# Optimization experiments

Hardware: AMD Instinct MI355X
Metric: run time of the kernel (lower is better)

Reference implementation:

```python
import jax, jax.numpy as jnp
import numpy as np
import math
from functools import partial

B = 256
H = 256
HEADS = 4
DK = H // HEADS
NA_MAX, NP_MAX, NH_MAX = 127, 23, 11


def _counts():
    i = np.arange(B)
    ac = (64 + i % 64).astype(np.int32)   # atoms per graph, 64..127
    pc = (8 + i % 16).astype(np.int32)    # pharm fragments per graph, 8..23
    hc = (4 + i % 8).astype(np.int32)     # hyper-edges per graph, 4..11
    return ac, pc, hc


def setup_inputs() -> dict:
    key = jax.random.key(0)
    ks = jax.random.split(key, 32)
    ac, pc, hc = _counts()
    na, npm, nh = int(ac.sum()), int(pc.sum()), int(hc.sum())
    w = 1.0 / math.sqrt(H)
    inp = {
        'atom_message': jax.random.normal(ks[0], (na, H), jnp.float32),
        'pharm_message': jax.random.normal(ks[1], (npm, H), jnp.float32),
        'hyper_message': jax.random.normal(ks[2], (nh, H), jnp.float32),
        'atom_counts': jnp.asarray(ac),
        'pharm_counts': jnp.asarray(pc),
        'hyper_counts': jnp.asarray(hc),
    }
    # two MultiHeadedAttention blocks: q/k/v/out linears each (W stored as [in, out])
    names = []
    for pre in ('p2h', 'a2p'):
        for part in ('Wq', 'bq', 'Wk', 'bk', 'Wv', 'bv', 'Wo', 'bo'):
            names.append(f'{pre}_{part}')
    ki = 3
    for n in names:
        if n.split('_')[1].startswith('W'):
            inp[n] = jax.random.normal(ks[ki], (H, H), jnp.float32) * w
        else:
            inp[n] = jax.random.normal(ks[ki], (H,), jnp.float32) * 0.01
        ki += 1
    # bidirectional GRU params, torch layout: W_ih [3H, H], W_hh [3H, H], b [3H]
    for d in ('f', 'b'):
        inp[f'gru_Wih_{d}'] = jax.random.normal(ks[ki], (3 * H, H), jnp.float32) * w; ki += 1
        inp[f'gru_Whh_{d}'] = jax.random.normal(ks[ki], (3 * H, H), jnp.float32) * w; ki += 1
        inp[f'gru_bih_{d}'] = jax.random.normal(ks[ki], (3 * H,), jnp.float32) * 0.01; ki += 1
        inp[f'gru_bhh_{d}'] = jax.random.normal(ks[ki], (3 * H,), jnp.float32) * 0.01; ki += 1
    return inp


def _split_pad(msg, counts, max_n):
    # faithful vectorized version of split_batch: narrow + zero-pad per graph
    starts = jnp.concatenate([jnp.zeros((1,), jnp.int32), jnp.cumsum(counts)[:-1].astype(jnp.int32)])
    j = jnp.arange(max_n)
    valid = j[None, :] < counts[:, None]                       # [B, max_n]
    idx = jnp.where(valid, starts[:, None] + j[None, :], msg.shape[0])
    padded_src = jnp.concatenate([msg, jnp.zeros((1, msg.shape[1]), msg.dtype)], 0)
    return padded_src[idx], valid                              # [B, max_n, H]


def _mha(q, k, v, mask, Wq, bq, Wk, bk, Wv, bv, Wo, bo):
    Bq, Lq, _ = q.shape
    def proj(x, W, b):
        y = x @ W + b
        return y.reshape(x.shape[0], x.shape[1], HEADS, DK).transpose(0, 2, 1, 3)
    qh, kh, vh = proj(q, Wq, bq), proj(k, Wk, bk), proj(v, Wv, bv)
    scores = jnp.einsum('bhqd,bhkd->bhqk', qh, kh) / math.sqrt(DK)
    scores = jnp.where(mask[:, None], jnp.float32(-1e9), scores)
    p = jax.nn.softmax(scores, axis=-1)
    o = jnp.einsum('bhqk,bhkd->bhqd', p, vh)
    o = o.transpose(0, 2, 1, 3).reshape(Bq, Lq, H)
    return o @ Wo + bo


def _gru_dir(x, h0, Wih, Whh, bih, bhh):
    # x: [B, T, H], torch GRU cell equations
    def step(h, xt):
        gi = xt @ Wih.T + bih
        gh = h @ Whh.T + bhh
        ir, iz, inn = jnp.split(gi, 3, axis=-1)
        hr, hz, hn = jnp.split(gh, 3, axis=-1)
        r = jax.nn.sigmoid(ir + hr)
        z = jax.nn.sigmoid(iz + hz)
        n = jnp.tanh(inn + r * hn)
        h = (1.0 - z) * n + z * h
        return h, h
    _, ys = jax.lax.scan(step, h0, x.transpose(1, 0, 2))
    return ys.transpose(1, 0, 2)


def reference(atom_message, pharm_message, hyper_message,
              p2h_Wq, p2h_bq, p2h_Wk, p2h_bk, p2h_Wv, p2h_bv, p2h_Wo, p2h_bo,
              a2p_Wq, a2p_bq, a2p_Wk, a2p_bk, a2p_Wv, a2p_bv, a2p_Wo, a2p_bo,
              gru_Wih_f, gru_Whh_f, gru_bih_f, gru_bhh_f,
              gru_Wih_b, gru_Whh_b, gru_bih_b, gru_bhh_b,
              atom_counts, pharm_counts, hyper_counts):
    atom_f, atom_valid = _split_pad(atom_message, atom_counts, NA_MAX)
    pharm_f, _ = _split_pad(pharm_message, pharm_counts, NP_MAX)
    hyper_f, _ = _split_pad(hyper_message, hyper_counts, NH_MAX)

    nz = lambda t: (t != 0).astype(jnp.float32)
    mask1 = jnp.einsum('bqh,bkh->bqk', nz(pharm_f), nz(hyper_f)) == 0  # [B, Np, Nh]
    mask2 = jnp.einsum('bqh,bkh->bqk', nz(atom_f), nz(pharm_f)) == 0   # [B, Na, Np]

    pharm_f = _mha(pharm_f, hyper_f, hyper_f, mask1,
                   p2h_Wq, p2h_bq, p2h_Wk, p2h_bk, p2h_Wv, p2h_bv, p2h_Wo, p2h_bo) + pharm_f
    h = _mha(atom_f, pharm_f, pharm_f, mask2,
             a2p_Wq, a2p_bq, a2p_Wk, a2p_bk, a2p_Wv, a2p_bv, a2p_Wo, a2p_bo) + atom_f

    h0 = h.max(axis=1)  # initial hidden per direction
    hf = _gru_dir(h, h0, gru_Wih_f, gru_Whh_f, gru_bih_f, gru_bhh_f)
    hb = _gru_dir(h[:, ::-1], h0, gru_Wih_b, gru_Whh_b, gru_bih_b, gru_bhh_b)[:, ::-1]
    hcat = jnp.concatenate([hf, hb], axis=-1)  # [B, Na, 2H]

    v = atom_valid.astype(hcat.dtype)[..., None]
    graph_embed = (hcat * v).sum(axis=1) / atom_counts[:, None].astype(hcat.dtype)
    return graph_embed  # [B, 2H]
```

## Files before the change

### kernel.cpp

```cpp
#include <hip/hip_runtime.h>
#include <hip/hip_fp16.h>
#include <math.h>

#define NB 256
#define HDIM 256
#define NHEADS 4
#define DKH 64
#define LA 127
#define LP 23
#define LH 11

typedef _Float16 h2v __attribute__((ext_vector_type(2)));
typedef _Float16 f16x8 __attribute__((ext_vector_type(8)));
typedef float f32x4 __attribute__((ext_vector_type(4)));
union F4H { float4 f4; h2v h[4]; };

__device__ __forceinline__ float dot2acc(h2v a, h2v b, float c) {
#if __has_builtin(__builtin_amdgcn_fdot2)
  return __builtin_amdgcn_fdot2(a, b, c, false);
#else
  return c + (float)a[0] * (float)b[0] + (float)a[1] * (float)b[1];
#endif
}

__device__ __forceinline__ float sigm(float x) { return 1.0f / (1.0f + __expf(-x)); }
__device__ __forceinline__ float tanh_fast(float x) { return 2.0f / (1.0f + __expf(-2.0f * x)) - 1.0f; }

__global__ void k_prep(const int* __restrict__ ac, const int* __restrict__ pc,
                       const int* __restrict__ hc, int* __restrict__ sa,
                       int* __restrict__ sp, int* __restrict__ sh,
                       const float* __restrict__ Whh_f, __half* __restrict__ Wh16_f,
                       const float* __restrict__ Whh_b, __half* __restrict__ Wh16_b,
                       const float* __restrict__ Wih_f, __half* __restrict__ Wf16_f,
                       const float* __restrict__ Wih_b, __half* __restrict__ Wf16_b,
                       const float* __restrict__ Wq, __half* __restrict__ Wqh,
                       __half* __restrict__ Wql, const float* __restrict__ Wo,
                       __half* __restrict__ Woh, __half* __restrict__ Wol) {
  const int NT = 768 * 256, NP = 256 * 256;
  if (blockIdx.x == gridDim.x - 1) {
    int t = threadIdx.x;
    if (t == 0) { int s = 0; for (int i = 0; i < NB; i++) { sa[i] = s; s += ac[i]; } }
    else if (t == 1) { int s = 0; for (int i = 0; i < NB; i++) { sp[i] = s; s += pc[i]; } }
    else if (t == 2) { int s = 0; for (int i = 0; i < NB; i++) { sh[i] = s; s += hc[i]; } }
    return;
  }
  int idx = blockIdx.x * 256 + threadIdx.x;
  if (idx < NT) { Wh16_f[idx] = __float2half(Whh_f[idx]); return; }
  idx -= NT;
  if (idx < NT) { Wh16_b[idx] = __float2half(Whh_b[idx]); return; }
  idx -= NT;
  if (idx < NT) {
    int u = idx & 7, lg = (idx >> 3) & 3, c = (idx >> 5) % 768, k0b = (idx >> 5) / 768;
    Wf16_f[idx] = __float2half(Wih_f[(size_t)c * 256 + k0b * 32 + lg * 8 + u]);
    return;
  }
  idx -= NT;
  if (idx < NT) {
    int u = idx & 7, lg = (idx >> 3) & 3, c = (idx >> 5) % 768, k0b = (idx >> 5) / 768;
    Wf16_b[idx] = __float2half(Wih_b[(size_t)c * 256 + k0b * 32 + lg * 8 + u]);
    return;
  }
  idx -= NT;
  if (idx < NP) {
    int u = idx & 7, lg = (idx >> 3) & 3, c = (idx >> 5) & 255, k0b = idx >> 13;
    float w = Wq[(size_t)(k0b * 32 + lg * 8 + u) * 256 + c];
    __half h = __float2half(w);
    Wqh[idx] = h; Wql[idx] = __float2half(w - __half2float(h));
    return;
  }
  idx -= NP;
  if (idx < NP) {
    int u = idx & 7, lg = (idx >> 3) & 3, c = (idx >> 5) & 255, k0b = idx >> 13;
    float w = Wo[(size_t)(k0b * 32 + lg * 8 + u) * 256 + c];
    __half h = __float2half(w);
    Woh[idx] = h; Wol[idx] = __float2half(w - __half2float(h));
  }
}

__global__ void k_gsplit(const float* __restrict__ msg, const int* __restrict__ starts,
                         const int* __restrict__ counts, int L, int M,
                         __half* __restrict__ hi, __half* __restrict__ lo) {
  int idx = blockIdx.x * blockDim.x + threadIdx.x;
  if (idx >= M * 256) return;
  int r = idx >> 8, c = idx & 255;
  int b = r / L, t = r - b * L;
  float v = (t < counts[b]) ? msg[(size_t)(starts[b] + t) * 256 + c] : 0.f;
  __half h = __float2half(v);
  hi[idx] = h;
  lo[idx] = __float2half(v - __half2float(h));
}

template <bool GATHER_A, bool RES_GATHER>
__global__ __launch_bounds__(256) void k_gemm(
    const float* __restrict__ A, const float* __restrict__ msg,
    const int* __restrict__ starts, const int* __restrict__ counts, int L,
    const float* __restrict__ W, const float* __restrict__ bias,
    const float* __restrict__ resmsg, float* __restrict__ C,
    __half* __restrict__ Ch, int N) {
  const int K = HDIM;
  __shared__ float As[16][76];
  __shared__ float Ws[16][72];
  int tid = threadIdx.x;
  int row0 = blockIdx.x * 64, col0 = blockIdx.y * 64;
  int arow = row0 + (tid >> 2);
  const float* asrc;
  if constexpr (GATHER_A) {
    int b = arow / L, t = arow - b * L;
    asrc = (t < counts[b]) ? (msg + (size_t)(starts[b] + t) * K) : nullptr;
  } else {
    asrc = A + (size_t)arow * K;
  }
  int ak = (tid & 3) * 4;
  int wk = tid >> 4, wn = (tid & 15) * 4;
  int ty = tid >> 4, tx = tid & 15;
  float acc[4][4] = {};
  for (int k0 = 0; k0 < K; k0 += 16) {
    float4 av = make_float4(0.f, 0.f, 0.f, 0.f);
    if (asrc) av = *(const float4*)(asrc + k0 + ak);
    float4 wv = *(const float4*)(W + (size_t)(k0 + wk) * N + col0 + wn);
    __syncthreads();
    int m = tid >> 2;
    As[ak + 0][m] = av.x; As[ak + 1][m] = av.y;
    As[ak + 2][m] = av.z; As[ak + 3][m] = av.w;
    *(float4*)&Ws[wk][wn] = wv;
    __syncthreads();
#pragma unroll
    for (int kk = 0; kk < 16; kk++) {
      float4 a = *(const float4*)&As[kk][ty * 4];
      float4 b = *(const float4*)&Ws[kk][tx * 4];
      acc[0][0] += a.x * b.x; acc[0][1] += a.x * b.y; acc[0][2] += a.x * b.z; acc[0][3] += a.x * b.w;
      acc[1][0] += a.y * b.x; acc[1][1] += a.y * b.y; acc[1][2] += a.y * b.z; acc[1][3] += a.y * b.w;
      acc[2][0] += a.z * b.x; acc[2][1] += a.z * b.y; acc[2][2] += a.z * b.z; acc[2][3] += a.z * b.w;
      acc[3][0] += a.w * b.x; acc[3][1] += a.w * b.y; acc[3][2] += a.w * b.z; acc[3][3] += a.w * b.w;
    }
  }
  float4 bv = *(const float4*)(bias + col0 + tx * 4);
#pragma unroll
  for (int i = 0; i < 4; i++) {
    int r = row0 + ty * 4 + i;
    float o0 = acc[i][0] + bv.x, o1 = acc[i][1] + bv.y,
          o2 = acc[i][2] + bv.z, o3 = acc[i][3] + bv.w;
    if constexpr (RES_GATHER) {
      int b = r / L, t = r - b * L;
      if (t < counts[b]) {
        float4 rv = *(const float4*)(resmsg + (size_t)(starts[b] + t) * K + col0 + tx * 4);
        o0 += rv.x; o1 += rv.y; o2 += rv.z; o3 += rv.w;
      }
    }
    size_t o = (size_t)r * N + col0 + tx * 4;
    *(float4*)(C + o) = make_float4(o0, o1, o2, o3);
    if (Ch) {
      Ch[o] = __float2half(o0); Ch[o + 1] = __float2half(o1);
      Ch[o + 2] = __float2half(o2); Ch[o + 3] = __float2half(o3);
    }
  }
}

template <bool GATHER_A>
__global__ __launch_bounds__(256) void k_gemm_kv(
    const float* __restrict__ A, const float* __restrict__ msg,
    const int* __restrict__ starts, const int* __restrict__ counts, int L,
    const float* __restrict__ W0, const float* __restrict__ b0, float* __restrict__ C0,
    const float* __restrict__ W1, const float* __restrict__ b1, float* __restrict__ C1) {
  const int K = HDIM, N = HDIM;
  const float* W = blockIdx.z ? W1 : W0;
  const float* bias = blockIdx.z ? b1 : b0;
  float* C = blockIdx.z ? C1 : C0;
  __shared__ float As[16][76];
  __shared__ float Ws[16][72];
  int tid = threadIdx.x;
  int row0 = blockIdx.x * 64, col0 = blockIdx.y * 64;
  int arow = row0 + (tid >> 2);
  const float* asrc;
  if constexpr (GATHER_A) {
    int b = arow / L, t = arow - b * L;
    asrc = (t < counts[b]) ? (msg + (size_t)(starts[b] + t) * K) : nullptr;
  } else {
    asrc = A + (size_t)arow * K;
  }
  int ak = (tid & 3) * 4;
  int wk = tid >> 4, wn = (tid & 15) * 4;
  int ty = tid >> 4, tx = tid & 15;
  float acc[4][4] = {};
  for (int k0 = 0; k0 < K; k0 += 16) {
    float4 av = make_float4(0.f, 0.f, 0.f, 0.f);
    if (asrc) av = *(const float4*)(asrc + k0 + ak);
    float4 wv = *(const float4*)(W + (size_t)(k0 + wk) * N + col0 + wn);
    __syncthreads();
    int m = tid >> 2;
    As[ak + 0][m] = av.x; As[ak + 1][m] = av.y;
    As[ak + 2][m] = av.z; As[ak + 3][m] = av.w;
    *(float4*)&Ws[wk][wn] = wv;
    __syncthreads();
#pragma unroll
    for (int kk = 0; kk < 16; kk++) {
      float4 a = *(const float4*)&As[kk][ty * 4];
      float4 b = *(const float4*)&Ws[kk][tx * 4];
      acc[0][0] += a.x * b.x; acc[0][1] += a.x * b.y; acc[0][2] += a.x * b.z; acc[0][3] += a.x * b.w;
      acc[1][0] += a.y * b.x; acc[1][1] += a.y * b.y; acc[1][2] += a.y * b.z; acc[1][3] += a.y * b.w;
      acc[2][0] += a.z * b.x; acc[2][1] += a.z * b.y; acc[2][2] += a.z * b.z; acc[2][3] += a.z * b.w;
      acc[3][0] += a.w * b.x; acc[3][1] += a.w * b.y; acc[3][2] += a.w * b.z; acc[3][3] += a.w * b.w;
    }
  }
  float4 bv = *(const float4*)(bias + col0 + tx * 4);
#pragma unroll
  for (int i = 0; i < 4; i++) {
    int r = row0 + ty * 4 + i;
    size_t o = (size_t)r * N + col0 + tx * 4;
    *(float4*)(C + o) = make_float4(acc[i][0] + bv.x, acc[i][1] + bv.y,
                                    acc[i][2] + bv.z, acc[i][3] + bv.w);
  }
}

template <bool RES>
__global__ __launch_bounds__(256) void k_mfma_sp(
    const __half* __restrict__ Ahi, const __half* __restrict__ Alo,
    const __half* __restrict__ Whi, const __half* __restrict__ Wlo,
    const float* __restrict__ bias, const float* __restrict__ resmsg,
    const int* __restrict__ starts, const int* __restrict__ counts, int L,
    float* __restrict__ Out, __half* __restrict__ Ch) {
  int w = threadIdx.x >> 6, l = threadIdx.x & 63;
  int row0 = blockIdx.x * 64 + w * 16;
  int col0 = blockIdx.y * 64;
  int lr = l & 15, lg = l >> 4;
  f32x4 acc[4] = {};
  const __half* ahrow = Ahi + (size_t)(row0 + lr) * 256 + lg * 8;
  const __half* alrow = Alo + (size_t)(row0 + lr) * 256 + lg * 8;
#pragma unroll
  for (int k0b = 0; k0b < 8; k0b++) {
    f16x8 ah = *(const f16x8*)(ahrow + k0b * 32);
    f16x8 al = *(const f16x8*)(alrow + k0b * 32);
#pragma unroll
    for (int nt = 0; nt < 4; nt++) {
      int c = col0 + nt * 16 + lr;
      size_t wi = ((size_t)(k0b * 256 + c) * 4 + lg) * 8;
      f16x8 bh = *(const f16x8*)(Whi + wi);
      f16x8 bl = *(const f16x8*)(Wlo + wi);
      acc[nt] = __builtin_amdgcn_mfma_f32_16x16x32_f16(ah, bh, acc[nt], 0, 0, 0);
      acc[nt] = __builtin_amdgcn_mfma_f32_16x16x32_f16(al, bh, acc[nt], 0, 0, 0);
      acc[nt] = __builtin_amdgcn_mfma_f32_16x16x32_f16(ah, bl, acc[nt], 0, 0, 0);
    }
  }
#pragma unroll
  for (int nt = 0; nt < 4; nt++) {
    int c = col0 + nt * 16 + lr;
    float bv = bias[c];
#pragma unroll
    for (int r = 0; r < 4; r++) {
      int row = row0 + lg * 4 + r;
      float o = acc[nt][r] + bv;
      if constexpr (RES) {
        int b = row / L, t = row - b * L;
        if (t < counts[b]) o += resmsg[(size_t)(starts[b] + t) * 256 + c];
      }
      size_t oidx = (size_t)row * 256 + c;
      Out[oidx] = o;
      if (Ch) Ch[oidx] = __float2half(o);
    }
  }
}

__global__ __launch_bounds__(256) void k_mfma_gi2(
    const __half* __restrict__ A16,
    const __half* __restrict__ Wf_f, const __half* __restrict__ Wf_b,
    const float* __restrict__ bias_f, const float* __restrict__ bias_b,
    __half* __restrict__ Out_f, __half* __restrict__ Out_b) {
  const int N = 768;
  int y = blockIdx.y;
  const __half* Wf = y < 12 ? Wf_f : Wf_b;
  const float* bias = y < 12 ? bias_f : bias_b;
  __half* Out = y < 12 ? Out_f : Out_b;
  int col0 = (y < 12 ? y : y - 12) * 64;
  int w = threadIdx.x >> 6, l = threadIdx.x & 63;
  int row0 = blockIdx.x * 64 + w * 16;
  int lr = l & 15, lg = l >> 4;
  f32x4 acc[4] = {};
  const __half* arow = A16 + (size_t)(row0 + lr) * 256 + lg * 8;
#pragma unroll
  for (int k0b = 0; k0b < 8; k0b++) {
    f16x8 a = *(const f16x8*)(arow + k0b * 32);
#pragma unroll
    for (int nt = 0; nt < 4; nt++) {
      int c = col0 + nt * 16 + lr;
      f16x8 b = *(const f16x8*)(Wf + ((size_t)(k0b * N + c) * 4 + lg) * 8);
      acc[nt] = __builtin_amdgcn_mfma_f32_16x16x32_f16(a, b, acc[nt], 0, 0, 0);
    }
  }
#pragma unroll
  for (int nt = 0; nt < 4; nt++) {
    int c = col0 + nt * 16 + lr;
    float bv = bias[c];
#pragma unroll
    for (int r = 0; r < 4; r++) {
      int row = row0 + lg * 4 + r;
      Out[(size_t)row * N + c] = __float2half(acc[nt][r] + bv);
    }
  }
}

template <int LQ, int LK, bool SPLITOUT>
__global__ __launch_bounds__(128) void k_attn(
    float* __restrict__ q, const float* __restrict__ kbuf,
    const float* __restrict__ vbuf, const int* __restrict__ cq,
    const int* __restrict__ ck, __half* __restrict__ oh, __half* __restrict__ ol) {
  __shared__ float qs[LQ][65];
  __shared__ float ks[LK][65];
  __shared__ float vs[LK][65];
  int b = blockIdx.x, head = blockIdx.y;
  int tid = threadIdx.x;
  for (int idx = tid; idx < LQ * 16; idx += 128) {
    int i = idx >> 4, c = (idx & 15) * 4;
    float4 v = *(const float4*)(q + (size_t)(b * LQ + i) * HDIM + head * DKH + c);
    qs[i][c] = v.x; qs[i][c + 1] = v.y; qs[i][c + 2] = v.z; qs[i][c + 3] = v.w;
  }
  for (int idx = tid; idx < LK * 16; idx += 128) {
    int i = idx >> 4, c = (idx & 15) * 4;
    float4 v = *(const float4*)(kbuf + (size_t)(b * LK + i) * HDIM + head * DKH + c);
    ks[i][c] = v.x; ks[i][c + 1] = v.y; ks[i][c + 2] = v.z; ks[i][c + 3] = v.w;
    float4 w = *(const float4*)(vbuf + (size_t)(b * LK + i) * HDIM + head * DKH + c);
    vs[i][c] = w.x; vs[i][c + 1] = w.y; vs[i][c + 2] = w.z; vs[i][c + 3] = w.w;
  }
  __syncthreads();
  int nq = cq[b], nk = ck[b];
  for (int i = tid; i < LQ; i += 128) {
    float4 qr[16];
#pragma unroll
    for (int c4 = 0; c4 < 16; c4++) qr[c4] = *(const float4*)&qs[i][c4 * 4];
    float s[LK];
    float mx = -INFINITY;
    bool qv = i < nq;
#pragma unroll
    for (int k = 0; k < LK; k++) {
      float d = -1e9f;
      if (qv && k < nk) {
        float acc = 0.f;
#pragma unroll
        for (int c4 = 0; c4 < 16; c4++) {
          float4 kv = *(const float4*)&ks[k][c4 * 4];
          acc += qr[c4].x * kv.x + qr[c4].y * kv.y + qr[c4].z * kv.z + qr[c4].w * kv.w;
        }
        d = acc * 0.125f;
      }
      s[k] = d;
      mx = fmaxf(mx, d);
    }
    float den = 0.f;
#pragma unroll
    for (int k = 0; k < LK; k++) { s[k] = expf(s[k] - mx); den += s[k]; }
    float inv = 1.0f / den;
#pragma unroll
    for (int c4 = 0; c4 < 16; c4++) {
      float4 a = make_float4(0.f, 0.f, 0.f, 0.f);
#pragma unroll
      for (int k = 0; k < LK; k++) {
        float4 vv = *(const float4*)&vs[k][c4 * 4];
        a.x += s[k] * vv.x; a.y += s[k] * vv.y;
        a.z += s[k] * vv.z; a.w += s[k] * vv.w;
      }
      a.x *= inv; a.y *= inv; a.z *= inv; a.w *= inv;
      size_t o = (size_t)(b * LQ + i) * HDIM + head * DKH + c4 * 4;
      *(float4*)(q + o) = a;
      if constexpr (SPLITOUT) {
        float vals[4] = {a.x, a.y, a.z, a.w};
#pragma unroll
        for (int u = 0; u < 4; u++) {
          __half h = __float2half(vals[u]);
          oh[o + u] = h;
          ol[o + u] = __float2half(vals[u] - __half2float(h));
        }
      }
    }
  }
}

__global__ __launch_bounds__(512, 2) void k_gru4(
    const float* __restrict__ h_x, const __half* __restrict__ Wh_f,
    const __half* __restrict__ Wh_b, const __half* __restrict__ gi_f,
    const __half* __restrict__ gi_b, const float* __restrict__ bhh_f,
    const float* __restrict__ bhh_b, const int* __restrict__ ac,
    float* __restrict__ out) {
  int bid = blockIdx.x;
  int dir = bid & 1, pair = bid >> 1;
  int g0 = pair, g1 = pair + 128;
  int tid = threadIdx.x;
  int j = tid >> 1, half = tid & 1;
  const __half* W = dir ? Wh_b : Wh_f;
  const __half* gih = dir ? gi_b : gi_f;
  const float* bhh = dir ? bhh_b : bhh_f;

  __shared__ float h0s[2][HDIM];
  {
    int g = tid >> 8, jj = tid & 255;
    int gg = g ? g1 : g0;
    const float* hp_ = h_x + (size_t)gg * LA * HDIM + jj;
    float m = -INFINITY;
    for (int t = 0; t < LA; t++) m = fmaxf(m, hp_[(size_t)t * HDIM]);
    h0s[g][jj] = m;
  }

  F4H wr[16], wz[16], wn[16];
  {
    const float4* Wr4 = (const float4*)(W + (size_t)j * 256 + half * 128);
    const float4* Wz4 = (const float4*)(W + (size_t)(256 + j) * 256 + half * 128);
    const float4* Wn4 = (const float4*)(W + (size_t)(512 + j) * 256 + half * 128);
#pragma unroll
    for (int p = 0; p < 16; p++) wr[p].f4 = Wr4[p];
#pragma unroll
    for (int p = 0; p < 16; p++) wz[p].f4 = Wz4[p];
#pragma unroll
    for (int p = 0; p < 16; p++) wn[p].f4 = Wn4[p];
  }
  float br = bhh[j], bz = bhh[256 + j], bn = bhh[512 + j];
  int cnt = ac[g0];

  __syncthreads();
  __shared__ __align__(16) __half hs[2][HDIM];
  float hprev0 = h0s[0][j];
  float hprev1 = h0s[1][j];
  if (half == 0) {
    hs[0][j] = __float2half(hprev0);
    hs[1][j] = __float2half(hprev1);
  }
  __syncthreads();

  const float4* h0p = (const float4*)hs[0] + half * 16;
  const float4* h1p = (const float4*)hs[1] + half * 16;
  float sum0 = 0.f, sum1 = 0.f;
  int nsteps = dir ? LA : cnt;
  for (int ti = 0; ti < nsteps; ti++) {
    int t = dir ? (LA - 1 - ti) : ti;
    const __half* gp0 = gih + ((size_t)g0 * LA + t) * 768 + j;
    const __half* gp1 = gih + ((size_t)g1 * LA + t) * 768 + j;
    float gr0 = __half2float(gp0[0]);
    float gz0 = __half2float(gp0[256]);
    float gn0 = __half2float(gp0[512]);
    float gr1 = __half2float(gp1[0]);
    float gz1 = __half2float(gp1[256]);
    float gn1 = __half2float(gp1[512]);
    float ap0 = 0.f, zp0 = 0.f, np0 = 0.f;
    float ap1 = 0.f, zp1 = 0.f, np1 = 0.f;
#pragma unroll
    for (int q = 0; q < 16; q++) {
      F4H hv0; hv0.f4 = h0p[q];
      F4H hv1; hv1.f4 = h1p[q];
#pragma unroll
      for (int u = 0; u < 4; u++) {
        ap0 = dot2acc(hv0.h[u], wr[q].h[u], ap0);
        zp0 = dot2acc(hv0.h[u], wz[q].h[u], zp0);
        np0 = dot2acc(hv0.h[u], wn[q].h[u], np0);
        ap1 = dot2acc(hv1.h[u], wr[q].h[u], ap1);
        zp1 = dot2acc(hv1.h[u], wz[q].h[u], zp1);
        np1 = dot2acc(hv1.h[u], wn[q].h[u], np1);
      }
    }
    ap0 += __shfl_xor(ap0, 1);
    zp0 += __shfl_xor(zp0, 1);
    np0 += __shfl_xor(np0, 1);
    ap1 += __shfl_xor(ap1, 1);
    zp1 += __shfl_xor(zp1, 1);
    np1 += __shfl_xor(np1, 1);
    float r0 = sigm(gr0 + br + ap0);
    float z0 = sigm(gz0 + bz + zp0);
    float n0 = tanh_fast(gn0 + bn + r0 * np0);
    float hnew0 = (1.f - z0) * n0 + z0 * hprev0;
    float r1 = sigm(gr1 + br + ap1);
    float z1 = sigm(gz1 + bz + zp1);
    float n1 = tanh_fast(gn1 + bn + r1 * np1);
    float hnew1 = (1.f - z1) * n1 + z1 * hprev1;
    __syncthreads();
    if (half == 0) {
      hs[0][j] = __float2half(hnew0);
      hs[1][j] = __float2half(hnew1);
    }
    hprev0 = hnew0;
    hprev1 = hnew1;
    if (t < cnt) { sum0 += hnew0; sum1 += hnew1; }
    __syncthreads();
  }
  if (half == 0) {
    out[(size_t)g0 * 512 + dir * 256 + j] = sum0 / (float)cnt;
    out[(size_t)g1 * 512 + dir * 256 + j] = sum1 / (float)cnt;
  }
}

extern "C" void kernel_launch(void* const* d_in, const int* in_sizes, int n_in,
                              void* d_out, int out_size, void* d_ws, size_t ws_size,
                              hipStream_t stream) {
  const float* atom_msg  = (const float*)d_in[0];
  const float* pharm_msg = (const float*)d_in[1];
  const float* hyper_msg = (const float*)d_in[2];
  const int* ac = (const int*)d_in[3];
  const int* pc = (const int*)d_in[4];
  const int* hc = (const int*)d_in[5];
  const float* p2h_Wq = (const float*)d_in[6];
  const float* p2h_bq = (const float*)d_in[7];
  const float* p2h_Wk = (const float*)d_in[8];
  const float* p2h_bk = (const float*)d_in[9];
  const float* p2h_Wv = (const float*)d_in[10];
  const float* p2h_bv = (const float*)d_in[11];
  const float* p2h_Wo = (const float*)d_in[12];
  const float* p2h_bo = (const float*)d_in[13];
  const float* a2p_Wq = (const float*)d_in[14];
  const float* a2p_bq = (const float*)d_in[15];
  const float* a2p_Wk = (const float*)d_in[16];
  const float* a2p_bk = (const float*)d_in[17];
  const float* a2p_Wv = (const float*)d_in[18];
  const float* a2p_bv = (const float*)d_in[19];
  const float* a2p_Wo = (const float*)d_in[20];
  const float* a2p_bo = (const float*)d_in[21];
  const float* Wih_f  = (const float*)d_in[22];
  const float* Whh_f  = (const float*)d_in[23];
  const float* bih_f  = (const float*)d_in[24];
  const float* bhh_f  = (const float*)d_in[25];
  const float* Wih_b  = (const float*)d_in[26];
  const float* Whh_b  = (const float*)d_in[27];
  const float* bih_b  = (const float*)d_in[28];
  const float* bhh_b  = (const float*)d_in[29];
  float* out = (float*)d_out;
  (void)in_sizes; (void)n_in; (void)out_size; (void)ws_size;

  char* wsb = (char*)d_ws;
  size_t off = 0;
  auto alloc = [&](size_t bytes) -> void* {
    void* p = wsb + off;
    off += (bytes + 255) & ~(size_t)255;
    return p;
  };
  const int MA = NB * LA, MP = NB * LP, MH = NB * LH;
  int* sa = (int*)alloc(NB * 4);
  int* sp = (int*)alloc(NB * 4);
  int* sh = (int*)alloc(NB * 4);
  __half* Wh16_f = (__half*)alloc((size_t)768 * 256 * 2);
  __half* Wh16_b = (__half*)alloc((size_t)768 * 256 * 2);
  __half* Wf16_f = (__half*)alloc((size_t)768 * 256 * 2);
  __half* Wf16_b = (__half*)alloc((size_t)768 * 256 * 2);
  __half* Wqh = (__half*)alloc((size_t)256 * 256 * 2);
  __half* Wql = (__half*)alloc((size_t)256 * 256 * 2);
  __half* Woh = (__half*)alloc((size_t)256 * 256 * 2);
  __half* Wol = (__half*)alloc((size_t)256 * 256 * 2);
  float* q_p = (float*)alloc((size_t)MP * HDIM * 4);
  float* k_h = (float*)alloc((size_t)MH * HDIM * 4);
  float* v_h = (float*)alloc((size_t)MH * HDIM * 4);
  float* ph2 = (float*)alloc((size_t)MP * HDIM * 4);
  float* q_a = (float*)alloc((size_t)MA * HDIM * 4);
  float* k_p = (float*)alloc((size_t)MP * HDIM * 4);
  float* v_p = (float*)alloc((size_t)MP * HDIM * 4);
  float* h_x = (float*)alloc((size_t)MA * HDIM * 4);
  __half* h_x16 = (__half*)alloc((size_t)MA * HDIM * 2);
  __half* gi_f = (__half*)alloc((size_t)MA * 768 * 2);
  __half* gi_b = (__half*)alloc((size_t)MA * 768 * 2);
  __half* Ah = gi_f;
  __half* Al = gi_f + (size_t)MA * HDIM;

  {
    const int NT = 768 * 256, NP = 256 * 256;
    int blocks = (4 * NT + 2 * NP) / 256 + 1;
    k_prep<<<blocks, 256, 0, stream>>>(ac, pc, hc, sa, sp, sh,
        Whh_f, Wh16_f, Whh_b, Wh16_b, Wih_f, Wf16_f, Wih_b, Wf16_b,
        a2p_Wq, Wqh, Wql, a2p_Wo, Woh, Wol);
  }
  k_gsplit<<<(MA * 256 + 255) / 256, 256, 0, stream>>>(atom_msg, sa, ac, LA, MA, Ah, Al);

  k_gemm<true, false><<<dim3(MP / 64, 4), 256, 0, stream>>>(
      nullptr, pharm_msg, sp, pc, LP, p2h_Wq, p2h_bq, nullptr, q_p, nullptr, 256);
  k_gemm_kv<true><<<dim3(MH / 64, 4, 2), 256, 0, stream>>>(
      nullptr, hyper_msg, sh, hc, LH, p2h_Wk, p2h_bk, k_h, p2h_Wv, p2h_bv, v_h);
  k_attn<LP, LH, false><<<dim3(NB, NHEADS), 128, 0, stream>>>(
      q_p, k_h, v_h, pc, hc, nullptr, nullptr);
  k_gemm<false, true><<<dim3(MP / 64, 4), 256, 0, stream>>>(
      q_p, nullptr, sp, pc, LP, p2h_Wo, p2h_bo, pharm_msg, ph2, nullptr, 256);

  k_mfma_sp<false><<<dim3(MA / 64, 4), 256, 0, stream>>>(
      Ah, Al, Wqh, Wql, a2p_bq, nullptr, nullptr, nullptr, 1, q_a, nullptr);
  k_gemm_kv<false><<<dim3(MP / 64, 4, 2), 256, 0, stream>>>(
      ph2, nullptr, nullptr, nullptr, 1, a2p_Wk, a2p_bk, k_p, a2p_Wv, a2p_bv, v_p);
  k_attn<LA, LP, true><<<dim3(NB, NHEADS), 128, 0, stream>>>(
      q_a, k_p, v_p, ac, pc, Ah, Al);
  k_mfma_sp<true><<<dim3(MA / 64, 4), 256, 0, stream>>>(
      Ah, Al, Woh, Wol, a2p_bo, atom_msg, sa, ac, LA, h_x, h_x16);

  k_mfma_gi2<<<dim3(MA / 64, 24), 256, 0, stream>>>(
      h_x16, Wf16_f, Wf16_b, bih_f, bih_b, gi_f, gi_b);
  k_gru4<<<NB, 512, 0, stream>>>(h_x, Wh16_f, Wh16_b, gi_f, gi_b, bhh_f, bhh_b, ac, out);
}
```

Before: 820.8 us.

## Fuse fp16 hi/lo split into MFMA GEMM loads and hoist GRU h0 max

Removes the separate gather-and-split kernel and the split-output path from attention. The split-precision MFMA kernel now reads fp32 activations directly, gathering atom rows when needed, and converts them to fp16 hi/lo in registers. The per-graph max for the GRU initial state moves out of the GRU kernel into a small standalone kernel. The attention inner loops are also simplified to scalar loops over LDS. This trades intermediate fp16 buffer traffic for extra per-tile conversion work. It also risks slower attention code, since the float4 register caching of the query row is gone.

Result: faster. 782.6 us (-4.7%).

```diff
diff --git a/kernel.cpp b/kernel.cpp
--- a/kernel.cpp
+++ b/kernel.cpp
@@ -75,19 +75,6 @@
     __half h = __float2half(w);
     Woh[idx] = h; Wol[idx] = __float2half(w - __half2float(h));
   }
-}
-
-__global__ void k_gsplit(const float* __restrict__ msg, const int* __restrict__ starts,
-                         const int* __restrict__ counts, int L, int M,
-                         __half* __restrict__ hi, __half* __restrict__ lo) {
-  int idx = blockIdx.x * blockDim.x + threadIdx.x;
-  if (idx >= M * 256) return;
-  int r = idx >> 8, c = idx & 255;
-  int b = r / L, t = r - b * L;
-  float v = (t < counts[b]) ? msg[(size_t)(starts[b] + t) * 256 + c] : 0.f;
-  __half h = __float2half(v);
-  hi[idx] = h;
-  lo[idx] = __float2half(v - __half2float(h));
 }
 
 template <bool GATHER_A, bool RES_GATHER>
@@ -212,24 +199,43 @@
   }
 }
 
-template <bool RES>
-__global__ __launch_bounds__(256) void k_mfma_sp(
-    const __half* __restrict__ Ahi, const __half* __restrict__ Alo,
+template <bool GATHER, bool RES>
+__global__ __launch_bounds__(256) void k_mfma_sp32(
+    const float* __restrict__ A, const float* __restrict__ msg,
+    const int* __restrict__ starts, const int* __restrict__ counts, int L,
     const __half* __restrict__ Whi, const __half* __restrict__ Wlo,
     const float* __restrict__ bias, const float* __restrict__ resmsg,
-    const int* __restrict__ starts, const int* __restrict__ counts, int L,
     float* __restrict__ Out, __half* __restrict__ Ch) {
   int w = threadIdx.x >> 6, l = threadIdx.x & 63;
   int row0 = blockIdx.x * 64 + w * 16;
   int col0 = blockIdx.y * 64;
   int lr = l & 15, lg = l >> 4;
+  int arow = row0 + lr;
+  const float* asrc;
+  if constexpr (GATHER) {
+    int b = arow / L, t = arow - b * L;
+    asrc = (t < counts[b]) ? (msg + (size_t)(starts[b] + t) * 256) : nullptr;
+  } else {
+    asrc = A + (size_t)arow * 256;
+  }
   f32x4 acc[4] = {};
-  const __half* ahrow = Ahi + (size_t)(row0 + lr) * 256 + lg * 8;
-  const __half* alrow = Alo + (size_t)(row0 + lr) * 256 + lg * 8;
 #pragma unroll
   for (int k0b = 0; k0b < 8; k0b++) {
-    f16x8 ah = *(const f16x8*)(ahrow + k0b * 32);
-    f16x8 al = *(const f16x8*)(alrow + k0b * 32);
+    f16x8 ah, al;
+    if (asrc) {
+      float av[8];
+      *(float4*)&av[0] = *(const float4*)(asrc + k0b * 32 + lg * 8);
+      *(float4*)&av[4] = *(const float4*)(asrc + k0b * 32 + lg * 8 + 4);
+#pragma unroll
+      for (int u = 0; u < 8; u++) {
+        _Float16 h = (_Float16)av[u];
+        ah[u] = h;
+        al[u] = (_Float16)(av[u] - (float)h);
+      }
+    } else {
+#pragma unroll
+      for (int u = 0; u < 8; u++) { ah[u] = (_Float16)0.f; al[u] = (_Float16)0.f; }
+    }
 #pragma unroll
     for (int nt = 0; nt < 4; nt++) {
       int c = col0 + nt * 16 + lr;
@@ -298,11 +304,11 @@
   }
 }
 
-template <int LQ, int LK, bool SPLITOUT>
+template <int LQ, int LK>
 __global__ __launch_bounds__(128) void k_attn(
     float* __restrict__ q, const float* __restrict__ kbuf,
     const float* __restrict__ vbuf, const int* __restrict__ cq,
-    const int* __restrict__ ck, __half* __restrict__ oh, __half* __restrict__ ol) {
+    const int* __restrict__ ck) {
   __shared__ float qs[LQ][65];
   __shared__ float ks[LK][65];
   __shared__ float vs[LK][65];
@@ -323,9 +329,6 @@
   __syncthreads();
   int nq = cq[b], nk = ck[b];
   for (int i = tid; i < LQ; i += 128) {
-    float4 qr[16];
-#pragma unroll
-    for (int c4 = 0; c4 < 16; c4++) qr[c4] = *(const float4*)&qs[i][c4 * 4];
     float s[LK];
     float mx = -INFINITY;
     bool qv = i < nq;
@@ -334,11 +337,7 @@
       float d = -1e9f;
       if (qv && k < nk) {
         float acc = 0.f;
-#pragma unroll
-        for (int c4 = 0; c4 < 16; c4++) {
-          float4 kv = *(const float4*)&ks[k][c4 * 4];
-          acc += qr[c4].x * kv.x + qr[c4].y * kv.y + qr[c4].z * kv.z + qr[c4].w * kv.w;
-        }
+        for (int c = 0; c < DKH; c++) acc += qs[i][c] * ks[k][c];
         d = acc * 0.125f;
       }
       s[k] = d;
@@ -348,33 +347,24 @@
 #pragma unroll
     for (int k = 0; k < LK; k++) { s[k] = expf(s[k] - mx); den += s[k]; }
     float inv = 1.0f / den;
-#pragma unroll
-    for (int c4 = 0; c4 < 16; c4++) {
-      float4 a = make_float4(0.f, 0.f, 0.f, 0.f);
-#pragma unroll
-      for (int k = 0; k < LK; k++) {
-        float4 vv = *(const float4*)&vs[k][c4 * 4];
-        a.x += s[k] * vv.x; a.y += s[k] * vv.y;
-        a.z += s[k] * vv.z; a.w += s[k] * vv.w;
-      }
-      a.x *= inv; a.y *= inv; a.z *= inv; a.w *= inv;
-      size_t o = (size_t)(b * LQ + i) * HDIM + head * DKH + c4 * 4;
-      *(float4*)(q + o) = a;
-      if constexpr (SPLITOUT) {
-        float vals[4] = {a.x, a.y, a.z, a.w};
-#pragma unroll
-        for (int u = 0; u < 4; u++) {
-          __half h = __float2half(vals[u]);
-          oh[o + u] = h;
-          ol[o + u] = __float2half(vals[u] - __half2float(h));
-        }
-      }
-    }
-  }
+    for (int c = 0; c < DKH; c++) {
+      float acc = 0.f;
+#pragma unroll
+      for (int k = 0; k < LK; k++) acc += s[k] * vs[k][c];
+      q[(size_t)(b * LQ + i) * HDIM + head * DKH + c] = acc * inv;
+    }
+  }
+}
+
+__global__ void k_rowmax(const float* __restrict__ h, float* __restrict__ h0) {
+  int b = blockIdx.x, j = threadIdx.x;
+  float m = -INFINITY;
+  for (int t = 0; t < LA; t++) m = fmaxf(m, h[((size_t)b * LA + t) * HDIM + j]);
+  h0[b * HDIM + j] = m;
 }
 
 __global__ __launch_bounds__(512, 2) void k_gru4(
-    const float* __restrict__ h_x, const __half* __restrict__ Wh_f,
+    const float* __restrict__ h0, const __half* __restrict__ Wh_f,
     const __half* __restrict__ Wh_b, const __half* __restrict__ gi_f,
     const __half* __restrict__ gi_b, const float* __restrict__ bhh_f,
     const float* __restrict__ bhh_b, const int* __restrict__ ac,
@@ -388,16 +378,6 @@
   const __half* gih = dir ? gi_b : gi_f;
   const float* bhh = dir ? bhh_b : bhh_f;
 
-  __shared__ float h0s[2][HDIM];
-  {
-    int g = tid >> 8, jj = tid & 255;
-    int gg = g ? g1 : g0;
-    const float* hp_ = h_x + (size_t)gg * LA * HDIM + jj;
-    float m = -INFINITY;
-    for (int t = 0; t < LA; t++) m = fmaxf(m, hp_[(size_t)t * HDIM]);
-    h0s[g][jj] = m;
-  }
-
   F4H wr[16], wz[16], wn[16];
   {
     const float4* Wr4 = (const float4*)(W + (size_t)j * 256 + half * 128);
@@ -413,10 +393,9 @@
   float br = bhh[j], bz = bhh[256 + j], bn = bhh[512 + j];
   int cnt = ac[g0];
 
-  __syncthreads();
   __shared__ __align__(16) __half hs[2][HDIM];
-  float hprev0 = h0s[0][j];
-  float hprev1 = h0s[1][j];
+  float hprev0 = h0[(size_t)g0 * HDIM + j];
+  float hprev1 = h0[(size_t)g1 * HDIM + j];
   if (half == 0) {
     hs[0][j] = __float2half(hprev0);
     hs[1][j] = __float2half(hprev1);
@@ -547,10 +526,9 @@
   float* v_p = (float*)alloc((size_t)MP * HDIM * 4);
   float* h_x = (float*)alloc((size_t)MA * HDIM * 4);
   __half* h_x16 = (__half*)alloc((size_t)MA * HDIM * 2);
+  float* h0  = (float*)alloc((size_t)NB * HDIM * 4);
   __half* gi_f = (__half*)alloc((size_t)MA * 768 * 2);
   __half* gi_b = (__half*)alloc((size_t)MA * 768 * 2);
-  __half* Ah = gi_f;
-  __half* Al = gi_f + (size_t)MA * HDIM;
 
   {
     const int NT = 768 * 256, NP = 256 * 256;
@@ -559,27 +537,25 @@
         Whh_f, Wh16_f, Whh_b, Wh16_b, Wih_f, Wf16_f, Wih_b, Wf16_b,
         a2p_Wq, Wqh, Wql, a2p_Wo, Woh, Wol);
   }
-  k_gsplit<<<(MA * 256 + 255) / 256, 256, 0, stream>>>(atom_msg, sa, ac, LA, MA, Ah, Al);
 
   k_gemm<true, false><<<dim3(MP / 64, 4), 256, 0, stream>>>(
       nullptr, pharm_msg, sp, pc, LP, p2h_Wq, p2h_bq, nullptr, q_p, nullptr, 256);
   k_gemm_kv<true><<<dim3(MH / 64, 4, 2), 256, 0, stream>>>(
       nullptr, hyper_msg, sh, hc, LH, p2h_Wk, p2h_bk, k_h, p2h_Wv, p2h_bv, v_h);
-  k_attn<LP, LH, false><<<dim3(NB, NHEADS), 128, 0, stream>>>(
-      q_p, k_h, v_h, pc, hc, nullptr, nullptr);
+  k_attn<LP, LH><<<dim3(NB, NHEADS), 128, 0, stream>>>(q_p, k_h, v_h, pc, hc);
   k_gemm<false, true><<<dim3(MP / 64, 4), 256, 0, stream>>>(
       q_p, nullptr, sp, pc, LP, p2h_Wo, p2h_bo, pharm_msg, ph2, nullptr, 256);
 
-  k_mfma_sp<false><<<dim3(MA / 64, 4), 256, 0, stream>>>(
-      Ah, Al, Wqh, Wql, a2p_bq, nullptr, nullptr, nullptr, 1, q_a, nullptr);
+  k_mfma_sp32<true, false><<<dim3(MA / 64, 4), 256, 0, stream>>>(
+      nullptr, atom_msg, sa, ac, LA, Wqh, Wql, a2p_bq, nullptr, q_a, nullptr);
   k_gemm_kv<false><<<dim3(MP / 64, 4, 2), 256, 0, stream>>>(
       ph2, nullptr, nullptr, nullptr, 1, a2p_Wk, a2p_bk, k_p, a2p_Wv, a2p_bv, v_p);
-  k_attn<LA, LP, true><<<dim3(NB, NHEADS), 128, 0, stream>>>(
-      q_a, k_p, v_p, ac, pc, Ah, Al);
-  k_mfma_sp<true><<<dim3(MA / 64, 4), 256, 0, stream>>>(
-      Ah, Al, Woh, Wol, a2p_bo, atom_msg, sa, ac, LA, h_x, h_x16);
-
+  k_attn<LA, LP><<<dim3(NB, NHEADS), 128, 0, stream>>>(q_a, k_p, v_p, ac, pc);
+  k_mfma_sp32<false, true><<<dim3(MA / 64, 4), 256, 0, stream>>>(
+      q_a, nullptr, sa, ac, LA, Woh, Wol, a2p_bo, atom_msg, h_x, h_x16);
+
+  k_rowmax<<<NB, 256, 0, stream>>>(h_x, h0);
   k_mfma_gi2<<<dim3(MA / 64, 24), 256, 0, stream>>>(
       h_x16, Wf16_f, Wf16_b, bih_f, bih_b, gi_f, gi_b);
-  k_gru4<<<NB, 512, 0, stream>>>(h_x, Wh16_f, Wh16_b, gi_f, gi_b, bhh_f, bhh_b, ac, out);
-}
+  k_gru4<<<NB, 512, 0, stream>>>(h0, Wh16_f, Wh16_b, gi_f, gi_b, bhh_f, bhh_b, ac, out);
+}
```
